# Kernel tuning notes

Measured on AMD Instinct MI355X. Metric: run time of the kernel, lower is better.

## Reference

```python
import jax, jax.numpy as jnp
import numpy as np

N, T, NC, D = 256, 20, 1, 32
NF, Q, VSTEPS, HDYN = 16, 32, 10, 256
HDIM = NF * 64           # n_filt * 4**3
DT = 0.1
BETA = 1.0
LOG2PI = float(np.log(2.0 * np.pi))


def conv2d(x, w, b):
    # k=4, s=2, p=1 : halves spatial dims. x: [B,Cin,H,W], w: [Cout,Cin,4,4]
    y = jax.lax.conv_general_dilated(x, w, (2, 2), [(1, 1), (1, 1)],
                                     dimension_numbers=('NCHW', 'OIHW', 'NCHW'))
    return y + b[None, :, None, None]


def deconv2d(x, w, b):
    # stride-2 transposed conv, doubles spatial dims. w: [Cout,Cin,4,4]
    y = jax.lax.conv_transpose(x, w, (2, 2), 'SAME',
                               dimension_numbers=('NCHW', 'OIHW', 'NCHW'))
    return y + b[None, :, None, None]


def encode(x, C1, c1, C2, c2, C3, c3, Wm, bm, Wl, bl):
    h = jax.nn.relu(conv2d(x, C1, c1))
    h = jax.nn.relu(conv2d(h, C2, c2))
    h = jax.nn.relu(conv2d(h, C3, c3))   # [B, 4*NF, 4, 4]
    h = h.reshape(h.shape[0], -1)        # [B, HDIM]
    return h @ Wm + bm, h @ Wl + bl


def setup_inputs() -> dict:
    key = jax.random.key(0)
    ks = jax.random.split(key, 40)
    r = lambda i, shape, s=0.05: s * jax.random.normal(ks[i], shape, jnp.float32)
    inp = {
        'X': jax.random.uniform(ks[0], (N, T, NC, D, D), jnp.float32),
        'eps_s0': jax.random.normal(ks[1], (N, Q), jnp.float32),
        'eps_v0': jax.random.normal(ks[2], (N, Q), jnp.float32),
        # enc_s (input = 1 frame)
        'Cs1': r(3, (NF, NC, 4, 4)), 'cs1': jnp.zeros((NF,)),
        'Cs2': r(4, (2 * NF, NF, 4, 4)), 'cs2': jnp.zeros((2 * NF,)),
        'Cs3': r(5, (4 * NF, 2 * NF, 4, 4)), 'cs3': jnp.zeros((4 * NF,)),
        'Wsm': r(6, (HDIM, Q)), 'bsm': jnp.zeros((Q,)),
        'Wsl': r(7, (HDIM, Q), 0.01), 'bsl': -1.0 * jnp.ones((Q,)),
        # enc_v (input = v_steps frames stacked as channels)
        'Cv1': r(8, (NF, VSTEPS * NC, 4, 4)), 'cv1': jnp.zeros((NF,)),
        'Cv2': r(9, (2 * NF, NF, 4, 4)), 'cv2': jnp.zeros((2 * NF,)),
        'Cv3': r(10, (4 * NF, 2 * NF, 4, 4)), 'cv3': jnp.zeros((4 * NF,)),
        'Wvm': r(11, (HDIM, Q)), 'bvm': jnp.zeros((Q,)),
        'Wvl': r(12, (HDIM, Q), 0.01), 'bvl': -1.0 * jnp.ones((Q,)),
        # dynamics f : R^{2q} -> R^q (tanh MLP)
        'W1': r(13, (2 * Q, HDYN), 0.1), 'b1': jnp.zeros((HDYN,)),
        'W2': r(14, (HDYN, Q), 0.1), 'b2': jnp.zeros((Q,)),
        # fc3 + decoder
        'Wf': r(15, (Q, HDIM)), 'bf': jnp.zeros((HDIM,)),
        'D1': r(16, (2 * NF, 4 * NF, 4, 4)), 'd1': jnp.zeros((2 * NF,)),
        'D2': r(17, (NF, 2 * NF, 4, 4)), 'd2': jnp.zeros((NF,)),
        'D3': r(18, (NC, NF, 4, 4)), 'd3': jnp.zeros((NC,)),
        'Ndata': 10000,
    }
    return inp


def reference(X, eps_s0, eps_v0,
              Cs1, cs1, Cs2, cs2, Cs3, cs3, Wsm, bsm, Wsl, bsl,
              Cv1, cv1, Cv2, cv2, Cv3, cv3, Wvm, bvm, Wvl, bvl,
              W1, b1, W2, b2, Wf, bf, D1, d1, D2, d2, D3, d3, Ndata):
    Nb, Tt = X.shape[0], X.shape[1]
    # ---- encode z0 = [v0, s0]
    s0_mu, s0_lv = encode(X[:, 0], Cs1, cs1, Cs2, cs2, Cs3, cs3, Wsm, bsm, Wsl, bsl)
    xv = X[:, :VSTEPS].reshape(Nb, VSTEPS * NC, D, D)
    v0_mu, v0_lv = encode(xv, Cv1, cv1, Cv2, cv2, Cv3, cv3, Wvm, bvm, Wvl, bvl)
    s0 = s0_mu + eps_s0 * jnp.exp(s0_lv)
    v0 = v0_mu + eps_v0 * jnp.exp(v0_lv)
    # standard-normal density of the base noise (q dims each)
    logp0 = (-0.5 * jnp.sum(eps_s0 ** 2, -1) - 0.5 * Q * LOG2PI) + \
            (-0.5 * jnp.sum(eps_v0 ** 2, -1) - 0.5 * Q * LOG2PI)
    z0 = jnp.concatenate([v0, s0], axis=1)               # [N,2q]
    qz0_m = jnp.concatenate([v0_mu, s0_mu], axis=1)
    qz0_logv = jnp.concatenate([v0_lv, s0_lv], axis=1)

    # ---- augmented ODE rhs: dz = [f(z), v], dlogp = -tr(df/dv)
    # exact trace for the tanh MLP: J = W2^T diag(1-h^2) W1^T, so
    # tr_{i<q} J = (1-h^2) @ c with c_k = sum_{i<q} W1[i,k] * W2[k,i]
    c = jnp.sum(W1[:Q] * W2.T, axis=0)                   # [HDYN]

    def rhs(vs):
        h = jnp.tanh(vs @ W1 + b1)                       # [N,HDYN]
        dv = h @ W2 + b2                                 # [N,q]
        dvs = jnp.concatenate([dv, vs[:, :Q]], axis=1)   # [N,2q]
        tr = (1.0 - h * h) @ c                           # [N]
        return dvs, -tr

    def rk4_step(carry, _):
        z, lp = carry
        k1z, k1l = rhs(z)
        k2z, k2l = rhs(z + 0.5 * DT * k1z)
        k3z, k3l = rhs(z + 0.5 * DT * k2z)
        k4z, k4l = rhs(z + DT * k3z)
        z2 = z + (DT / 6.0) * (k1z + 2 * k2z + 2 * k3z + k4z)
        lp2 = lp + (DT / 6.0) * (k1l + 2 * k2l + 2 * k3l + k4l)
        return (z2, lp2), (z2, lp2)

    (_, _), (zs, lps) = jax.lax.scan(rk4_step, (z0, logp0), None, length=Tt - 1)
    zt = jnp.concatenate([z0[None], zs], axis=0)         # [T,N,2q]
    logp = jnp.concatenate([logp0[None], lps], axis=0)   # [T,N]
    ztL = jnp.transpose(zt, (1, 0, 2))[None]             # [1,N,T,2q] (L=1)
    logpL = logp.T[None]                                 # [1,N,T]

    # ---- decode positions s_t
    s = ztL[..., Q:].reshape(-1, Q) @ Wf + bf            # [N*T, HDIM]
    h = s.reshape(-1, 4 * NF, 4, 4)
    h = jax.nn.relu(deconv2d(h, D1, d1))                 # [N*T,2NF,8,8]
    h = jax.nn.relu(deconv2d(h, D2, d2))                 # [N*T,NF,16,16]
    Xrec = jax.nn.sigmoid(deconv2d(h, D3, d3))           # [N*T,NC,32,32]
    Xrec = Xrec.reshape(1, Nb, Tt, NC, D, D)

    # ---- ELBO
    log_pzt = -0.5 * jnp.sum(ztL ** 2, -1) - Q * LOG2PI  # N(0,I) over 2q dims
    kl_z = (logpL - log_pzt).sum(2).mean(0)              # [N]
    lhood_L = jnp.log(0.001 + Xrec) * X[None] + jnp.log(1.001 - Xrec) * (1.0 - X[None])
    lhood = lhood_L.sum((2, 3, 4, 5)).mean(0)            # [N]
    kl_w = 0.5 * (jnp.sum(W1 ** 2) + jnp.sum(W2 ** 2))
    Nd = jnp.float32(Ndata)
    lh = Nd * lhood.mean()
    klz = Nd * kl_z.mean()
    elbo = lh - klz - BETA * kl_w
    return Xrec, qz0_m, qz0_logv, ztL, elbo, lh, klz, BETA * kl_w


if __name__ == '__main__':
    outs = reference(**setup_inputs())
    print(outs[0].shape, float(outs[4]))
```

## Files before the change

### kernel.cpp

```cpp
#include <hip/hip_runtime.h>
#include <math.h>

#define N_S 256
#define T_S 20
#define D_S 32
#define NF_S 16
#define Q_S 32
#define HDYN_S 256
#define HDIM_S 1024
#define VSTEPS_S 10
#define DT_S 0.1f
#define LOG2PI_F 1.8378770664093453f

#define OUT_XREC 0
#define OUT_QM   5242880
#define OUT_QLV  5259264
#define OUT_ZT   5275648
#define OUT_SCAL 5603328

#define OS_A1S   0
#define OS_A2S   1048576
#define OS_A3S   1572864

#define WS_A1V   0
#define WS_A3V   0
#define WS_WT2   32768
#define WS_WT3   40960
#define WS_A2V   1048576
#define WS_M1    1048576
#define WS_C1    1114112
#define WS_S0MU  1572864
#define WS_S0LV  1581056
#define WS_V0MU  1589248
#define WS_V0LV  1597440
#define WS_LOGP  1605632
#define WS_LHOOD 1610752
#define WS_KLZ   1611008
#define WS_KLW   1611264
#define WS_TC    1611520
#define TC_S1 (WS_TC + 0)
#define TC_V1 (WS_TC + 256)
#define TC_S2 (WS_TC + 2816)
#define TC_V2 (WS_TC + 11008)
#define TC_S3 (WS_TC + 19200)
#define TC_V3 (WS_TC + 51968)

__device__ inline void enc_tr(const float* __restrict__ src, float* __restrict__ dst,
                              int e, int CI, int CO) {
    int co = e % CO; int r = e / CO; int tap = r & 15; int ci = r >> 4;
    dst[e] = src[(co * CI + ci) * 16 + tap];
}
__device__ inline void dec_tr(const float* __restrict__ src, float* __restrict__ dst,
                              int e, int CI, int CO) {
    int co = e % CO; int r = e / CO; int ci = r % CI; int tap = r / CI;
    dst[e] = src[(co * CI + ci) * 16 + tap];
}

__global__ __launch_bounds__(256) void prep_enc(
    const float* __restrict__ Cs1, const float* __restrict__ Cv1,
    const float* __restrict__ Cs2, const float* __restrict__ Cv2,
    const float* __restrict__ Cs3, const float* __restrict__ Cv3,
    float* __restrict__ ws)
{
    int idx = blockIdx.x * 256 + threadIdx.x;
    if (blockIdx.x == 0) ws[WS_LHOOD + threadIdx.x] = 0.f;
    if (idx < 256)        enc_tr(Cs1, ws + TC_S1, idx,          1, 16);
    else if (idx < 2816)  enc_tr(Cv1, ws + TC_V1, idx - 256,   10, 16);
    else if (idx < 11008) enc_tr(Cs2, ws + TC_S2, idx - 2816,  16, 32);
    else if (idx < 19200) enc_tr(Cv2, ws + TC_V2, idx - 11008, 16, 32);
    else if (idx < 51968) enc_tr(Cs3, ws + TC_S3, idx - 19200, 32, 64);
    else if (idx < 84736) enc_tr(Cv3, ws + TC_V3, idx - 51968, 32, 64);
}

__global__ __launch_bounds__(256) void conv1_both(
    const float* __restrict__ x,
    const float* __restrict__ wts, const float* __restrict__ bs, float* __restrict__ outs,
    const float* __restrict__ wtv, const float* __restrict__ bv, float* __restrict__ outv)
{
    __shared__ float xin[10 * 630];
    int sel = blockIdx.z;
    int cin = sel ? 10 : 1;
    const float* wt = sel ? wtv : wts;
    const float* bias = sel ? bv : bs;
    float* out = sel ? outv : outs;

    int b = blockIdx.x, yh = blockIdx.y, t = threadIdx.x;
    for (int e = t; e < cin * 576; e += 256) {
        int ci = e / 576;
        int r = (e >> 5) - ci * 18;
        int cx = e & 31;
        int gy = yh * 16 - 1 + r;
        float v = (gy >= 0 && gy < 32) ? x[(size_t)b * 20480 + ci * 1024 + gy * 32 + cx] : 0.f;
        xin[ci * 630 + r * 35 + cx + 1] = v;
    }
    for (int e = t; e < cin * 18; e += 256) {
        int ci = e / 18, r = e - ci * 18;
        xin[ci * 630 + r * 35 + 0] = 0.f;
        xin[ci * 630 + r * 35 + 33] = 0.f;
    }
    __syncthreads();

    int ocq = __builtin_amdgcn_readfirstlane(t >> 7);
    int p = t & 127;
    int oyl = p >> 4, ox = p & 15;
    const float* wg = wt + ocq * 8;
    float acc[8];
    #pragma unroll
    for (int j = 0; j < 8; j++) acc[j] = bias[ocq * 8 + j];
    for (int ci = 0; ci < cin; ci++) {
        const float* xc = xin + ci * 630;
        const float* wc = wg + ci * 256;
        #pragma unroll
        for (int ky = 0; ky < 4; ky++) {
            const float* xr = xc + (2 * oyl + ky) * 35;
            #pragma unroll
            for (int kx = 0; kx < 4; kx++) {
                float v = xr[2 * ox + kx];
                const float4* w4 = (const float4*)(wc + (ky * 4 + kx) * 16);
                float4 wa = w4[0], wb2 = w4[1];
                acc[0] = fmaf(v, wa.x, acc[0]);
                acc[1] = fmaf(v, wa.y, acc[1]);
                acc[2] = fmaf(v, wa.z, acc[2]);
                acc[3] = fmaf(v, wa.w, acc[3]);
                acc[4] = fmaf(v, wb2.x, acc[4]);
                acc[5] = fmaf(v, wb2.y, acc[5]);
                acc[6] = fmaf(v, wb2.z, acc[6]);
                acc[7] = fmaf(v, wb2.w, acc[7]);
            }
        }
    }
    int oy = yh * 8 + oyl;
    size_t ob = (size_t)b * 4096 + (size_t)(ocq * 8) * 256 + oy * 16 + ox;
    #pragma unroll
    for (int j = 0; j < 8; j++) out[ob + (size_t)j * 256] = fmaxf(acc[j], 0.f);
}

__global__ __launch_bounds__(256) void conv2_both(
    const float* __restrict__ a1s, const float* __restrict__ wts, const float* __restrict__ bsb,
    float* __restrict__ outs,
    const float* __restrict__ a1v, const float* __restrict__ wtv, const float* __restrict__ bvb,
    float* __restrict__ outv)
{
    __shared__ float xin[16 * 272];
    int sel = blockIdx.z;
    const float* a1 = sel ? a1v : a1s;
    const float* wt = sel ? wtv : wts;
    const float* bias = sel ? bvb : bsb;
    float* out = sel ? outv : outs;

    int b = blockIdx.x, h = blockIdx.y, t = threadIdx.x;
    for (int e = t; e < 4096; e += 256) {
        int ci = e >> 8, r = e & 255, iy = r >> 4, ix = r & 15;
        xin[ci * 272 + iy * 17 + ix] = a1[(size_t)b * 4096 + e];
    }
    __syncthreads();

    int ocq = __builtin_amdgcn_readfirstlane(t >> 6);
    int p = t & 63;
    int pa = p >> 3, pb = p & 7;
    int hbase = h * 16 + ocq * 4;
    float acc[4];
    #pragma unroll
    for (int j = 0; j < 4; j++) acc[j] = bias[hbase + j];
    for (int ci = 0; ci < 16; ci++) {
        const float* xc = xin + ci * 272;
        const float* wc = wt + ci * 512 + hbase;
        #pragma unroll
        for (int ky = 0; ky < 4; ky++) {
            int iy = 2 * pa - 1 + ky;
            if ((unsigned)iy >= 16u) continue;
            const float* xr = xc + iy * 17;
            #pragma unroll
            for (int kx = 0; kx < 4; kx++) {
                int ix = 2 * pb - 1 + kx;
                if ((unsigned)ix >= 16u) continue;
                float v = xr[ix];
                float4 wv = *(const float4*)(wc + (ky * 4 + kx) * 32);
                acc[0] = fmaf(v, wv.x, acc[0]);
                acc[1] = fmaf(v, wv.y, acc[1]);
                acc[2] = fmaf(v, wv.z, acc[2]);
                acc[3] = fmaf(v, wv.w, acc[3]);
            }
        }
    }
    size_t ob = (size_t)b * 2048 + (size_t)(hbase) * 64 + pa * 8 + pb;
    #pragma unroll
    for (int j = 0; j < 4; j++) out[ob + (size_t)j * 64] = fmaxf(acc[j], 0.f);
}

__global__ __launch_bounds__(256) void conv3_both(
    const float* __restrict__ a2s, const float* __restrict__ wts, const float* __restrict__ bsb,
    float* __restrict__ outs,
    const float* __restrict__ a2v, const float* __restrict__ wtv, const float* __restrict__ bvb,
    float* __restrict__ outv)
{
    __shared__ float xin[32 * 72];
    __shared__ float wl[16384];
    __shared__ float bl[32];
    int sel = blockIdx.z;
    const float* a2 = sel ? a2v : a2s;
    const float* wt = sel ? wtv : wts;
    const float* bias = sel ? bvb : bsb;
    float* out = sel ? outv : outs;

    int b = blockIdx.x, h = blockIdx.y, t = threadIdx.x;
    for (int e = t; e < 2048; e += 256) {
        int ci = e >> 6, r = e & 63, iy = r >> 3, ix = r & 7;
        xin[ci * 72 + iy * 9 + ix] = a2[(size_t)b * 2048 + e];
    }
    for (int e4 = t; e4 < 4096; e4 += 256) {
        int grp = e4 >> 3, c4 = e4 & 7;
        ((float4*)wl)[e4] = ((const float4*)(wt + grp * 64 + h * 32))[c4];
    }
    if (t < 32) bl[t] = bias[h * 32 + t];
    __syncthreads();

    int ocq = t >> 4, p = t & 15;
    int pa = p >> 2, pb = p & 3;
    float a0 = bl[ocq * 2], a1 = bl[ocq * 2 + 1];
    for (int ci = 0; ci < 32; ci++) {
        const float* xc = xin + ci * 72;
        const float* wc = wl + ci * 512 + ocq * 2;
        #pragma unroll
        for (int ky = 0; ky < 4; ky++) {
            int iy = 2 * pa - 1 + ky;
            if ((unsigned)iy >= 8u) continue;
            const float* xr = xc + iy * 9;
            #pragma unroll
            for (int kx = 0; kx < 4; kx++) {
                int ix = 2 * pb - 1 + kx;
                if ((unsigned)ix >= 8u) continue;
                float v = xr[ix];
                float2 wv = *(const float2*)(wc + (ky * 4 + kx) * 32);
                a0 = fmaf(v, wv.x, a0);
                a1 = fmaf(v, wv.y, a1);
            }
        }
    }
    size_t ob = (size_t)b * 1024 + (size_t)(h * 32 + ocq * 2) * 16 + pa * 4 + pb;
    out[ob] = fmaxf(a0, 0.f);
    out[ob + 16] = fmaxf(a1, 0.f);
}

__global__ __launch_bounds__(256) void fc_both(
    const float* __restrict__ hs, const float* __restrict__ hv,
    const float* __restrict__ Wsm, const float* __restrict__ bsm,
    const float* __restrict__ Wsl, const float* __restrict__ bsl,
    const float* __restrict__ Wvm, const float* __restrict__ bvm,
    const float* __restrict__ Wvl, const float* __restrict__ bvl,
    float* __restrict__ mus, float* __restrict__ lvs,
    float* __restrict__ muv, float* __restrict__ lvv)
{
    __shared__ float pm[8][32], pl[8][32];
    int sel = blockIdx.x >> 8;
    int b = blockIdx.x & 255, t = threadIdx.x;
    const float* h  = sel ? hv : hs;
    const float* Wm = sel ? Wvm : Wsm;
    const float* bm = sel ? bvm : bsm;
    const float* Wl = sel ? Wvl : Wsl;
    const float* bl = sel ? bvl : bsl;
    float* mu = sel ? muv : mus;
    float* lv = sel ? lvv : lvs;

    int q = t & 31, c = t >> 5;
    const float* hb = h + (size_t)b * HDIM_S + c * 128;
    const float* wmp = Wm + (c * 128) * Q_S + q;
    const float* wlp = Wl + (c * 128) * Q_S + q;
    float am = 0.f, al = 0.f;
    #pragma unroll 4
    for (int k = 0; k < 128; k++) {
        float hv2 = hb[k];
        am = fmaf(hv2, wmp[k * Q_S], am);
        al = fmaf(hv2, wlp[k * Q_S], al);
    }
    pm[c][q] = am; pl[c][q] = al;
    __syncthreads();
    if (t < 32) {
        float s = bm[t];
        #pragma unroll
        for (int c2 = 0; c2 < 8; c2++) s += pm[c2][t];
        mu[b * Q_S + t] = s;
    } else if (t < 64) {
        int qq = t - 32;
        float s = bl[qq];
        #pragma unroll
        for (int c2 = 0; c2 < 8; c2++) s += pl[c2][qq];
        lv[b * Q_S + qq] = s;
    }
}

__global__ __launch_bounds__(256) void reparam_prep(
    const float* __restrict__ s0mu, const float* __restrict__ s0lv,
    const float* __restrict__ v0mu, const float* __restrict__ v0lv,
    const float* __restrict__ eps_s, const float* __restrict__ eps_v,
    const float* __restrict__ Wf, const float* __restrict__ bf,
    const float* __restrict__ D1, const float* __restrict__ d1,
    const float* __restrict__ D2, const float* __restrict__ D3,
    float* __restrict__ ws,
    float* __restrict__ qm, float* __restrict__ qlv,
    float* __restrict__ ztL, float* __restrict__ logp)
{
    __shared__ float shA[4096];
    __shared__ float shB[4096];
    int n = blockIdx.x, t = threadIdx.x;

    if (n < 64) {
        int j = n >> 3, q4 = n & 7;
        for (int e = t; e < 4096; e += 256) {
            int qq = e >> 10, k = e & 1023;
            shA[e] = Wf[(size_t)(q4 * 4 + qq) * 1024 + k];
        }
        for (int e = t; e < 4096; e += 256) {
            int ocg = e >> 10, r = e & 1023;
            shB[e] = D1[(size_t)(ocg * 8 + j) * 1024 + r];
        }
        __syncthreads();
        int p = t & 63, ocg = t >> 6;
        int y = p >> 3, x = p & 7;
        float acc[4] = {0.f, 0.f, 0.f, 0.f};
        #pragma unroll
        for (int sy = 0; sy < 2; sy++) {
            int ky = (y & 1) + 2 * sy;
            int iy = ((y + ky) >> 1) - 1;
            if ((unsigned)iy >= 4u) continue;
            #pragma unroll
            for (int sx = 0; sx < 2; sx++) {
                int kx = (x & 1) + 2 * sx;
                int ix = ((x + kx) >> 1) - 1;
                if ((unsigned)ix >= 4u) continue;
                const float* dl = shB + ocg * 1024 + ky * 4 + kx;
                const float* wl = shA + iy * 4 + ix;
                for (int ci = 0; ci < 64; ci++) {
                    float wv = dl[ci * 16];
                    int kb = ci * 16;
                    acc[0] = fmaf(wl[kb],        wv, acc[0]);
                    acc[1] = fmaf(wl[1024 + kb], wv, acc[1]);
                    acc[2] = fmaf(wl[2048 + kb], wv, acc[2]);
                    acc[3] = fmaf(wl[3072 + kb], wv, acc[3]);
                }
            }
        }
        ((float4*)(ws + WS_M1))[n * 256 + t] = make_float4(acc[0], acc[1], acc[2], acc[3]);
    } else if (n < 80) {
        int bb = n - 64;
        for (int e = t; e < 1024; e += 256) shA[e] = bf[e];
        for (int e = t; e < 2048; e += 256) shB[e] = D1[(size_t)bb * 2048 + e];
        __syncthreads();
        int oidx = t >> 1, half = t & 1;
        int ocr = oidx >> 6, p = oidx & 63;
        int y = p >> 3, x = p & 7;
        float acc = 0.f;
        #pragma unroll
        for (int sy = 0; sy < 2; sy++) {
            int ky = (y & 1) + 2 * sy;
            int iy = ((y + ky) >> 1) - 1;
            if ((unsigned)iy >= 4u) continue;
            #pragma unroll
            for (int sx = 0; sx < 2; sx++) {
                int kx = (x & 1) + 2 * sx;
                int ix = ((x + kx) >> 1) - 1;
                if ((unsigned)ix >= 4u) continue;
                const float* dl = shB + ocr * 1024 + half * 512 + ky * 4 + kx;
                const float* wl = shA + half * 512 + iy * 4 + ix;
                for (int cc = 0; cc < 32; cc++)
                    acc = fmaf(wl[cc * 16], dl[cc * 16], acc);
            }
        }
        acc += __shfl_down(acc, 1, 64);
        if (half == 0) {
            int oc = bb * 2 + ocr;
            ws[WS_C1 + (oc & 7) * 256 + (oc >> 3) * 64 + p] = acc + d1[oc];
        }
    } else if (n < 113) {
        int idx = (n - 80) * 256 + t;
        if (idx < 8192)      dec_tr(D2, ws + WS_WT2, idx,        32, 16);
        else if (idx < 8448) dec_tr(D3, ws + WS_WT3, idx - 8192, 16, 1);
    }

    if (t < 64) {
        int q = t & 31;
        float mu, lvv2, ep;
        if (t < 32) { mu = v0mu[n*32+q]; lvv2 = v0lv[n*32+q]; ep = eps_v[n*32+q]; }
        else        { mu = s0mu[n*32+q]; lvv2 = s0lv[n*32+q]; ep = eps_s[n*32+q]; }
        float zv = fmaf(ep, expf(lvv2), mu);
        qm[n*64 + t]  = mu;
        qlv[n*64 + t] = lvv2;
        ztL[(size_t)n * T_S * 64 + t] = zv;
        float e2 = ep * ep;
        #pragma unroll
        for (int off = 32; off; off >>= 1) e2 += __shfl_down(e2, off, 64);
        if (t == 0) logp[n * T_S] = -0.5f * e2 - Q_S * LOG2PI_F;
    }
}

__global__ __launch_bounds__(256) void ode_kernel(
    const float* __restrict__ W1, const float* __restrict__ b1,
    const float* __restrict__ W2, const float* __restrict__ b2,
    float* __restrict__ ztL, const float* __restrict__ logp,
    float* __restrict__ klz)
{
    __shared__ float W2s[HDYN_S * Q_S];
    __shared__ float zeval[64];
    __shared__ float hsh[HDYN_S];
    __shared__ float dvred[HDYN_S];
    __shared__ float red4[4];
    int n = blockIdx.x;
    int t = threadIdx.x;

    for (int i = t; i < HDYN_S * Q_S; i += 256) W2s[i] = W2[i];
    float w1r[64];
    #pragma unroll
    for (int j = 0; j < 64; j++) w1r[j] = W1[j * HDYN_S + t];
    float b1r = b1[t];
    __syncthreads();
    float ck = 0.f;
    #pragma unroll
    for (int i = 0; i < Q_S; i++) ck = fmaf(w1r[i], W2s[t * Q_S + i], ck);

    size_t zoff = (size_t)n * T_S * 64;
    float zj = 0.f, ksumj = 0.f, zevalj = 0.f, lp = 0.f, lsum = 0.f, klacc = 0.f;
    if (t < 64) { zj = ztL[zoff + t]; zevalj = zj; zeval[t] = zj; }
    if (t == 0) lp = logp[n * T_S];

    if (t < 64) {
        float e2 = zj * zj;
        #pragma unroll
        for (int off = 32; off; off >>= 1) e2 += __shfl_down(e2, off, 64);
        if (t == 0) klacc += lp - (-0.5f * e2 - Q_S * LOG2PI_F);
    }

    const float wc[4] = {1.f, 2.f, 2.f, 1.f};
    const float ac[3] = {0.5f * DT_S, 0.5f * DT_S, DT_S};

    for (int step = 1; step < T_S; step++) {
        for (int e = 0; e < 4; e++) {
            __syncthreads();
            float p0 = 0.f, p1 = 0.f, p2 = 0.f, p3 = 0.f;
            #pragma unroll
            for (int j = 0; j < 16; j++) {
                p0 = fmaf(zeval[j],      w1r[j],      p0);
                p1 = fmaf(zeval[j + 16], w1r[j + 16], p1);
                p2 = fmaf(zeval[j + 32], w1r[j + 32], p2);
                p3 = fmaf(zeval[j + 48], w1r[j + 48], p3);
            }
            float pre = b1r + ((p0 + p1) + (p2 + p3));
            float hk = tanhf(pre);
            hsh[t] = hk;
            float gk = (1.f - hk * hk) * ck;
            #pragma unroll
            for (int off = 32; off; off >>= 1) gk += __shfl_down(gk, off, 64);
            if ((t & 63) == 0) red4[t >> 6] = gk;
            __syncthreads();
            {
                int i = t & 31, p = t >> 5;
                float a0 = 0.f, a1 = 0.f;
                #pragma unroll
                for (int kk = 0; kk < 16; kk++) {
                    a0 = fmaf(hsh[p * 32 + kk],      W2s[(p * 32 + kk) * Q_S + i],      a0);
                    a1 = fmaf(hsh[p * 32 + 16 + kk], W2s[(p * 32 + 16 + kk) * Q_S + i], a1);
                }
                dvred[t] = a0 + a1;
            }
            __syncthreads();
            if (t < 64) {
                float tr = red4[0] + red4[1] + red4[2] + red4[3];
                float zv_shfl = __shfl(zevalj, (t >= 32) ? (t - 32) : t, 64);
                float kzv;
                if (t < 32) {
                    float dvi = b2[t];
                    #pragma unroll
                    for (int p = 0; p < 8; p++) dvi += dvred[p * 32 + t];
                    kzv = dvi;
                } else kzv = zv_shfl;
                if (e == 0) ksumj = kzv; else ksumj = fmaf(wc[e], kzv, ksumj);
                if (t == 0) { float kl = -tr; lsum = (e == 0) ? kl : fmaf(wc[e], kl, lsum); }
                if (e < 3) {
                    zevalj = fmaf(ac[e], kzv, zj);
                    zeval[t] = zevalj;
                } else {
                    zj = fmaf(DT_S / 6.f, ksumj, zj);
                    zevalj = zj; zeval[t] = zj;
                    ztL[zoff + step * 64 + t] = zj;
                    if (t == 0) lp = fmaf(DT_S / 6.f, lsum, lp);
                    float e2 = zj * zj;
                    #pragma unroll
                    for (int off = 32; off; off >>= 1) e2 += __shfl_down(e2, off, 64);
                    if (t == 0) klacc += lp - (-0.5f * e2 - Q_S * LOG2PI_F);
                }
            }
        }
    }
    if (t == 0) klz[n] = klacc;
}

__global__ __launch_bounds__(256) void decoder5(
    const float* __restrict__ ztL, const float* __restrict__ M1L, const float* __restrict__ c1L,
    const float* __restrict__ wt2, const float* __restrict__ d2,
    const float* __restrict__ wt3, const float* __restrict__ d3,
    const float* __restrict__ X, float* __restrict__ Xrec, float* __restrict__ lhood)
{
    __shared__ float zs[32];
    __shared__ float regA[3600];
    __shared__ float regB[4160];
    __shared__ float sh4[4];
    float* h2f = regB;
    float* h1f = regA;
    float* xst = regA;
    const int bidx = blockIdx.x;
    const int t = threadIdx.x;
    const int wu = __builtin_amdgcn_readfirstlane(t >> 6);
    const int l = t & 63;
    const int py = wu >> 1, px = wu & 1;

    if (t < 32) zs[t] = ztL[(size_t)bidx * 64 + 32 + t];
    {
        float4 z4 = make_float4(0.f, 0.f, 0.f, 0.f);
        for (int e = t; e < 900; e += 256) ((float4*)regA)[e] = z4;
    }
    __syncthreads();

    {
        float acc[8];
        #pragma unroll
        for (int j = 0; j < 8; j++) acc[j] = c1L[j * 256 + t];
        const float4* M14 = (const float4*)M1L;
        #pragma unroll
        for (int q4 = 0; q4 < 8; q4++) {
            float4 z4 = *(const float4*)(zs + q4 * 4);
            #pragma unroll
            for (int j = 0; j < 8; j++) {
                float4 m = M14[(j * 8 + q4) * 256 + t];
                acc[j] = fmaf(z4.x, m.x, fmaf(z4.y, m.y, fmaf(z4.z, m.z, fmaf(z4.w, m.w, acc[j]))));
            }
        }
        int p = t & 63, ocg = t >> 6;
        int y = p >> 3, x = p & 7;
        float* hp = h1f + (y + 1) * 360 + (x + 1) * 36 + ocg * 8;
        float4 r0, r1;
        r0.x = fmaxf(acc[0], 0.f); r0.y = fmaxf(acc[1], 0.f);
        r0.z = fmaxf(acc[2], 0.f); r0.w = fmaxf(acc[3], 0.f);
        r1.x = fmaxf(acc[4], 0.f); r1.y = fmaxf(acc[5], 0.f);
        r1.z = fmaxf(acc[6], 0.f); r1.w = fmaxf(acc[7], 0.f);
        *(float4*)(hp)     = r0;
        *(float4*)(hp + 4) = r1;
    }
    __syncthreads();

    {
        int a = l >> 3, b = l & 7;
        float acc[16];
        #pragma unroll
        for (int j = 0; j < 16; j++) acc[j] = d2[j];
        #pragma unroll
        for (int sy = 0; sy < 2; sy++) {
            int ky = py + 2 * sy;
            int iyf = a + py + sy - 1;
            #pragma unroll
            for (int sx = 0; sx < 2; sx++) {
                int kx = px + 2 * sx;
                int ixf = b + px + sx - 1;
                const float4* ip4 = (const float4*)(h1f + (iyf + 1) * 360 + (ixf + 1) * 36);
                const float* wb = wt2 + (ky * 4 + kx) * 512;
                #pragma unroll 2
                for (int cc = 0; cc < 8; cc++) {
                    float4 v = ip4[cc];
                    float vv[4] = {v.x, v.y, v.z, v.w};
                    #pragma unroll
                    for (int r = 0; r < 4; r++) {
                        const float4* wq = (const float4*)(wb + (cc * 4 + r) * 16);
                        float4 w0 = wq[0], w1 = wq[1], w2 = wq[2], w3 = wq[3];
                        float vr = vv[r];
                        acc[0]  = fmaf(vr, w0.x, acc[0]);
                        acc[1]  = fmaf(vr, w0.y, acc[1]);
                        acc[2]  = fmaf(vr, w0.z, acc[2]);
                        acc[3]  = fmaf(vr, w0.w, acc[3]);
                        acc[4]  = fmaf(vr, w1.x, acc[4]);
                        acc[5]  = fmaf(vr, w1.y, acc[5]);
                        acc[6]  = fmaf(vr, w1.z, acc[6]);
                        acc[7]  = fmaf(vr, w1.w, acc[7]);
                        acc[8]  = fmaf(vr, w2.x, acc[8]);
                        acc[9]  = fmaf(vr, w2.y, acc[9]);
                        acc[10] = fmaf(vr, w2.z, acc[10]);
                        acc[11] = fmaf(vr, w2.w, acc[11]);
                        acc[12] = fmaf(vr, w3.x, acc[12]);
                        acc[13] = fmaf(vr, w3.y, acc[13]);
                        acc[14] = fmaf(vr, w3.z, acc[14]);
                        acc[15] = fmaf(vr, w3.w, acc[15]);
                    }
                }
            }
        }
        float* hq = h2f + (2 * a + py) * 260 + (2 * b + px) * 16;
        #pragma unroll
        for (int j = 0; j < 4; j++) {
            float4 r;
            r.x = fmaxf(acc[j*4+0], 0.f);
            r.y = fmaxf(acc[j*4+1], 0.f);
            r.z = fmaxf(acc[j*4+2], 0.f);
            r.w = fmaxf(acc[j*4+3], 0.f);
            *(float4*)(hq + j * 4) = r;
        }
    }
    __syncthreads();

    {
        int oy2 = l >> 2, b3 = l & 3;
        float acc[4];
        float d30 = d3[0];
        #pragma unroll
        for (int k = 0; k < 4; k++) acc[k] = d30;
        #pragma unroll
        for (int sy = 0; sy < 2; sy++) {
            int ky = py + 2 * sy;
            int iy = oy2 + py + sy - 1;
            if ((unsigned)iy >= 16u) continue;
            #pragma unroll
            for (int sx = 0; sx < 2; sx++) {
                int kx = px + 2 * sx;
                int cx = px + sx - 1;
                const float* wvp = wt3 + (ky * 4 + kx) * 16;
                #pragma unroll
                for (int k = 0; k < 4; k++) {
                    int ix = b3 + 4 * k + cx;
                    if ((unsigned)ix >= 16u) continue;
                    const float4* in4 = (const float4*)(h2f + iy * 260 + ix * 16);
                    #pragma unroll
                    for (int cc = 0; cc < 4; cc++) {
                        float4 v = in4[cc];
                        float4 wq = ((const float4*)wvp)[cc];
                        acc[k] = fmaf(v.x, wq.x, acc[k]);
                        acc[k] = fmaf(v.y, wq.y, acc[k]);
                        acc[k] = fmaf(v.z, wq.z, acc[k]);
                        acc[k] = fmaf(v.w, wq.w, acc[k]);
                    }
                }
            }
        }
        int oy = 2 * oy2 + py;
        #pragma unroll
        for (int k = 0; k < 4; k++) {
            int ox = 2 * (b3 + 4 * k) + px;
            xst[oy * 36 + ox] = 1.f / (1.f + expf(-acc[k]));
        }
    }
    __syncthreads();

    {
        int row = t >> 3, col = (t & 7) * 4;
        float4 xr4 = *(const float4*)(xst + row * 36 + col);
        *(float4*)(Xrec + (size_t)bidx * 1024 + t * 4) = xr4;
        float4 xi4 = *(const float4*)(X + (size_t)bidx * 1024 + t * 4);
        float ll = 0.f;
        ll += logf(0.001f + xr4.x) * xi4.x + logf(1.001f - xr4.x) * (1.f - xi4.x);
        ll += logf(0.001f + xr4.y) * xi4.y + logf(1.001f - xr4.y) * (1.f - xi4.y);
        ll += logf(0.001f + xr4.z) * xi4.z + logf(1.001f - xr4.z) * (1.f - xi4.z);
        ll += logf(0.001f + xr4.w) * xi4.w + logf(1.001f - xr4.w) * (1.f - xi4.w);
        #pragma unroll
        for (int off = 32; off; off >>= 1) ll += __shfl_down(ll, off, 64);
        if ((t & 63) == 0) sh4[t >> 6] = ll;
    }
    __syncthreads();
    if (t == 0) atomicAdd(&lhood[bidx / T_S], sh4[0] + sh4[1] + sh4[2] + sh4[3]);
}

__global__ __launch_bounds__(256) void final2(
    const float* __restrict__ lhood, const float* __restrict__ klz,
    const float* __restrict__ W1, const float* __restrict__ W2,
    const int* __restrict__ Ndata, float* __restrict__ outs)
{
    __shared__ float shA[4], shB[4], shC[4];
    int t = threadIdx.x;
    float a = lhood[t];
    float b = klz[t];
    float c = 0.f;
    for (int i = t; i < 64 * HDYN_S; i += 256) c = fmaf(W1[i], W1[i], c);
    for (int i = t; i < HDYN_S * Q_S; i += 256) c = fmaf(W2[i], W2[i], c);
    #pragma unroll
    for (int off = 32; off; off >>= 1) {
        a += __shfl_down(a, off, 64);
        b += __shfl_down(b, off, 64);
        c += __shfl_down(c, off, 64);
    }
    if ((t & 63) == 0) { shA[t >> 6] = a; shB[t >> 6] = b; shC[t >> 6] = c; }
    __syncthreads();
    if (t == 0) {
        float Nd = (float)Ndata[0];
        float lh = Nd * ((shA[0] + shA[1] + shA[2] + shA[3]) / 256.f);
        float kz = Nd * ((shB[0] + shB[1] + shB[2] + shB[3]) / 256.f);
        float bkw = 0.5f * (shC[0] + shC[1] + shC[2] + shC[3]);
        outs[0] = lh - kz - bkw;
        outs[1] = lh;
        outs[2] = kz;
        outs[3] = bkw;
    }
}

extern "C" void kernel_launch(void* const* d_in, const int* in_sizes, int n_in,
                              void* d_out, int out_size, void* d_ws, size_t ws_size,
                              hipStream_t stream) {
    const float* X      = (const float*)d_in[0];
    const float* eps_s0 = (const float*)d_in[1];
    const float* eps_v0 = (const float*)d_in[2];
    const float* Cs1 = (const float*)d_in[3],  *cs1 = (const float*)d_in[4];
    const float* Cs2 = (const float*)d_in[5],  *cs2 = (const float*)d_in[6];
    const float* Cs3 = (const float*)d_in[7],  *cs3 = (const float*)d_in[8];
    const float* Wsm = (const float*)d_in[9],  *bsm = (const float*)d_in[10];
    const float* Wsl = (const float*)d_in[11], *bsl = (const float*)d_in[12];
    const float* Cv1 = (const float*)d_in[13], *cv1 = (const float*)d_in[14];
    const float* Cv2 = (const float*)d_in[15], *cv2 = (const float*)d_in[16];
    const float* Cv3 = (const float*)d_in[17], *cv3 = (const float*)d_in[18];
    const float* Wvm = (const float*)d_in[19], *bvm = (const float*)d_in[20];
    const float* Wvl = (const float*)d_in[21], *bvl = (const float*)d_in[22];
    const float* W1  = (const float*)d_in[23], *b1  = (const float*)d_in[24];
    const float* W2  = (const float*)d_in[25], *b2  = (const float*)d_in[26];
    const float* Wf  = (const float*)d_in[27], *bf  = (const float*)d_in[28];
    const float* D1  = (const float*)d_in[29], *d1  = (const float*)d_in[30];
    const float* D2  = (const float*)d_in[31], *d2  = (const float*)d_in[32];
    const float* D3  = (const float*)d_in[33], *d3  = (const float*)d_in[34];
    const int*   Ndata = (const int*)d_in[35];

    float* out = (float*)d_out;
    float* ws  = (float*)d_ws;

    float* a1s = out + OS_A1S;
    float* a2s = out + OS_A2S;
    float* a3s = out + OS_A3S;

    prep_enc<<<331, 256, 0, stream>>>(Cs1, Cv1, Cs2, Cv2, Cs3, Cv3, ws);

    conv1_both<<<dim3(256, 2, 2), 256, 0, stream>>>(X,
        ws + TC_S1, cs1, a1s,
        ws + TC_V1, cv1, ws + WS_A1V);
    conv2_both<<<dim3(256, 2, 2), 256, 0, stream>>>(
        a1s, ws + TC_S2, cs2, a2s,
        ws + WS_A1V, ws + TC_V2, cv2, ws + WS_A2V);
    conv3_both<<<dim3(256, 2, 2), 256, 0, stream>>>(
        a2s, ws + TC_S3, cs3, a3s,
        ws + WS_A2V, ws + TC_V3, cv3, ws + WS_A3V);
    fc_both<<<512, 256, 0, stream>>>(a3s, ws + WS_A3V,
        Wsm, bsm, Wsl, bsl, Wvm, bvm, Wvl, bvl,
        ws + WS_S0MU, ws + WS_S0LV, ws + WS_V0MU, ws + WS_V0LV);

    reparam_prep<<<256, 256, 0, stream>>>(ws + WS_S0MU, ws + WS_S0LV, ws + WS_V0MU, ws + WS_V0LV,
                                          eps_s0, eps_v0, Wf, bf, D1, d1, D2, D3, ws,
                                          out + OUT_QM, out + OUT_QLV,
                                          out + OUT_ZT, ws + WS_LOGP);

    ode_kernel<<<256, 256, 0, stream>>>(W1, b1, W2, b2, out + OUT_ZT, ws + WS_LOGP,
                                        ws + WS_KLZ);

    decoder5<<<5120, 256, 0, stream>>>(out + OUT_ZT, ws + WS_M1, ws + WS_C1,
                                       ws + WS_WT2, d2, ws + WS_WT3, d3,
                                       X, out + OUT_XREC, ws + WS_LHOOD);

    final2<<<1, 256, 0, stream>>>(ws + WS_LHOOD, ws + WS_KLZ, W1, W2, Ndata,
                                  out + OUT_SCAL);
}
```

Baseline: 495.3 us.

## Fuse conv3 with FC heads and fold reparam/decoder prep into ODE launch

```diff
diff --git a/kernel.cpp b/kernel.cpp
--- a/kernel.cpp
+++ b/kernel.cpp
@@ -20,10 +20,8 @@
 
 #define OS_A1S   0
 #define OS_A2S   1048576
-#define OS_A3S   1572864
 
 #define WS_A1V   0
-#define WS_A3V   0
 #define WS_WT2   32768
 #define WS_WT3   40960
 #define WS_A2V   1048576
@@ -33,10 +31,8 @@
 #define WS_S0LV  1581056
 #define WS_V0MU  1589248
 #define WS_V0LV  1597440
-#define WS_LOGP  1605632
 #define WS_LHOOD 1610752
 #define WS_KLZ   1611008
-#define WS_KLW   1611264
 #define WS_TC    1611520
 #define TC_S1 (WS_TC + 0)
 #define TC_V1 (WS_TC + 256)
@@ -62,14 +58,20 @@
     const float* __restrict__ Cs3, const float* __restrict__ Cv3,
     float* __restrict__ ws)
 {
-    int idx = blockIdx.x * 256 + threadIdx.x;
-    if (blockIdx.x == 0) ws[WS_LHOOD + threadIdx.x] = 0.f;
-    if (idx < 256)        enc_tr(Cs1, ws + TC_S1, idx,          1, 16);
-    else if (idx < 2816)  enc_tr(Cv1, ws + TC_V1, idx - 256,   10, 16);
-    else if (idx < 11008) enc_tr(Cs2, ws + TC_S2, idx - 2816,  16, 32);
-    else if (idx < 19200) enc_tr(Cv2, ws + TC_V2, idx - 11008, 16, 32);
-    else if (idx < 51968) enc_tr(Cs3, ws + TC_S3, idx - 19200, 32, 64);
-    else if (idx < 84736) enc_tr(Cv3, ws + TC_V3, idx - 51968, 32, 64);
+    int blk = blockIdx.x, t = threadIdx.x;
+    if (blk < 331) {
+        int idx = blk * 256 + t;
+        if (blk == 0) ws[WS_LHOOD + t] = 0.f;
+        if (idx < 256)        enc_tr(Cs1, ws + TC_S1, idx,          1, 16);
+        else if (idx < 2816)  enc_tr(Cv1, ws + TC_V1, idx - 256,   10, 16);
+        else if (idx < 11008) enc_tr(Cs2, ws + TC_S2, idx - 2816,  16, 32);
+        else if (idx < 19200) enc_tr(Cv2, ws + TC_V2, idx - 11008, 16, 32);
+        else if (idx < 51968) enc_tr(Cs3, ws + TC_S3, idx - 19200, 32, 64);
+        else if (idx < 84736) enc_tr(Cv3, ws + TC_V3, idx - 51968, 32, 64);
+    } else {
+        int zi = (blk - 331) * 256 + t;
+        ws[WS_S0MU + zi] = 0.f;
+    }
 }
 
 __global__ __launch_bounds__(256) void conv1_both(
@@ -188,20 +190,25 @@
     for (int j = 0; j < 4; j++) out[ob + (size_t)j * 64] = fmaxf(acc[j], 0.f);
 }
 
-__global__ __launch_bounds__(256) void conv3_both(
-    const float* __restrict__ a2s, const float* __restrict__ wts, const float* __restrict__ bsb,
-    float* __restrict__ outs,
-    const float* __restrict__ a2v, const float* __restrict__ wtv, const float* __restrict__ bvb,
-    float* __restrict__ outv)
+__global__ __launch_bounds__(256) void conv3fc_both(
+    const float* __restrict__ a2s, const float* __restrict__ wts,
+    const float* __restrict__ bsb,
+    const float* __restrict__ Wsm, const float* __restrict__ Wsl,
+    float* __restrict__ mus, float* __restrict__ lvs,
+    const float* __restrict__ a2v, const float* __restrict__ wtv,
+    const float* __restrict__ bvb,
+    const float* __restrict__ Wvm, const float* __restrict__ Wvl,
+    float* __restrict__ muv, float* __restrict__ lvv)
 {
     __shared__ float xin[32 * 72];
     __shared__ float wl[16384];
     __shared__ float bl[32];
+    __shared__ float hbuf[512];
+    __shared__ float pr[256];
     int sel = blockIdx.z;
     const float* a2 = sel ? a2v : a2s;
     const float* wt = sel ? wtv : wts;
     const float* bias = sel ? bvb : bsb;
-    float* out = sel ? outv : outs;
 
     int b = blockIdx.x, h = blockIdx.y, t = threadIdx.x;
     for (int e = t; e < 2048; e += 256) {
@@ -237,167 +244,43 @@
             }
         }
     }
-    size_t ob = (size_t)b * 1024 + (size_t)(h * 32 + ocq * 2) * 16 + pa * 4 + pb;
-    out[ob] = fmaxf(a0, 0.f);
-    out[ob + 16] = fmaxf(a1, 0.f);
-}
-
-__global__ __launch_bounds__(256) void fc_both(
-    const float* __restrict__ hs, const float* __restrict__ hv,
-    const float* __restrict__ Wsm, const float* __restrict__ bsm,
-    const float* __restrict__ Wsl, const float* __restrict__ bsl,
-    const float* __restrict__ Wvm, const float* __restrict__ bvm,
-    const float* __restrict__ Wvl, const float* __restrict__ bvl,
-    float* __restrict__ mus, float* __restrict__ lvs,
-    float* __restrict__ muv, float* __restrict__ lvv)
-{
-    __shared__ float pm[8][32], pl[8][32];
-    int sel = blockIdx.x >> 8;
-    int b = blockIdx.x & 255, t = threadIdx.x;
-    const float* h  = sel ? hv : hs;
-    const float* Wm = sel ? Wvm : Wsm;
-    const float* bm = sel ? bvm : bsm;
-    const float* Wl = sel ? Wvl : Wsl;
-    const float* bl = sel ? bvl : bsl;
-    float* mu = sel ? muv : mus;
-    float* lv = sel ? lvv : lvs;
-
-    int q = t & 31, c = t >> 5;
-    const float* hb = h + (size_t)b * HDIM_S + c * 128;
-    const float* wmp = Wm + (c * 128) * Q_S + q;
-    const float* wlp = Wl + (c * 128) * Q_S + q;
-    float am = 0.f, al = 0.f;
-    #pragma unroll 4
-    for (int k = 0; k < 128; k++) {
-        float hv2 = hb[k];
-        am = fmaf(hv2, wmp[k * Q_S], am);
-        al = fmaf(hv2, wlp[k * Q_S], al);
-    }
-    pm[c][q] = am; pl[c][q] = al;
-    __syncthreads();
-    if (t < 32) {
-        float s = bm[t];
-        #pragma unroll
-        for (int c2 = 0; c2 < 8; c2++) s += pm[c2][t];
-        mu[b * Q_S + t] = s;
-    } else if (t < 64) {
-        int qq = t - 32;
-        float s = bl[qq];
-        #pragma unroll
-        for (int c2 = 0; c2 < 8; c2++) s += pl[c2][qq];
-        lv[b * Q_S + qq] = s;
-    }
-}
-
-__global__ __launch_bounds__(256) void reparam_prep(
-    const float* __restrict__ s0mu, const float* __restrict__ s0lv,
-    const float* __restrict__ v0mu, const float* __restrict__ v0lv,
+    int lp_ = ocq * 32 + p;
+    hbuf[lp_]      = fmaxf(a0, 0.f);
+    hbuf[lp_ + 16] = fmaxf(a1, 0.f);
+    __syncthreads();
+
+    {
+        int q = t & 63, c = t >> 6, qq = q & 31;
+        const float* Wb = (q < 32) ? (sel ? Wvm : Wsm) : (sel ? Wvl : Wsl);
+        const float* wp = Wb + (size_t)(h * 512 + c * 128) * 32 + qq;
+        const float* hp = hbuf + c * 128;
+        float s = 0.f;
+        #pragma unroll 4
+        for (int k = 0; k < 128; k++) s = fmaf(hp[k], wp[(size_t)k * 32], s);
+        pr[c * 64 + q] = s;
+    }
+    __syncthreads();
+    if (t < 64) {
+        float s = (pr[t] + pr[64 + t]) + (pr[128 + t] + pr[192 + t]);
+        float* dst = (t < 32) ? (sel ? muv : mus) : (sel ? lvv : lvs);
+        atomicAdd(&dst[b * 32 + (t & 31)], s);
+    }
+}
+
+__global__ __launch_bounds__(256) void ode_kernel(
+    const float* __restrict__ W1, const float* __restrict__ b1,
+    const float* __restrict__ W2, const float* __restrict__ b2,
+    const float* __restrict__ s0mu_a, const float* __restrict__ s0lv_a,
+    const float* __restrict__ v0mu_a, const float* __restrict__ v0lv_a,
+    const float* __restrict__ bsm, const float* __restrict__ bsl,
+    const float* __restrict__ bvm, const float* __restrict__ bvl,
     const float* __restrict__ eps_s, const float* __restrict__ eps_v,
     const float* __restrict__ Wf, const float* __restrict__ bf,
     const float* __restrict__ D1, const float* __restrict__ d1,
     const float* __restrict__ D2, const float* __restrict__ D3,
     float* __restrict__ ws,
     float* __restrict__ qm, float* __restrict__ qlv,
-    float* __restrict__ ztL, float* __restrict__ logp)
-{
-    __shared__ float shA[4096];
-    __shared__ float shB[4096];
-    int n = blockIdx.x, t = threadIdx.x;
-
-    if (n < 64) {
-        int j = n >> 3, q4 = n & 7;
-        for (int e = t; e < 4096; e += 256) {
-            int qq = e >> 10, k = e & 1023;
-            shA[e] = Wf[(size_t)(q4 * 4 + qq) * 1024 + k];
-        }
-        for (int e = t; e < 4096; e += 256) {
-            int ocg = e >> 10, r = e & 1023;
-            shB[e] = D1[(size_t)(ocg * 8 + j) * 1024 + r];
-        }
-        __syncthreads();
-        int p = t & 63, ocg = t >> 6;
-        int y = p >> 3, x = p & 7;
-        float acc[4] = {0.f, 0.f, 0.f, 0.f};
-        #pragma unroll
-        for (int sy = 0; sy < 2; sy++) {
-            int ky = (y & 1) + 2 * sy;
-            int iy = ((y + ky) >> 1) - 1;
-            if ((unsigned)iy >= 4u) continue;
-            #pragma unroll
-            for (int sx = 0; sx < 2; sx++) {
-                int kx = (x & 1) + 2 * sx;
-                int ix = ((x + kx) >> 1) - 1;
-                if ((unsigned)ix >= 4u) continue;
-                const float* dl = shB + ocg * 1024 + ky * 4 + kx;
-                const float* wl = shA + iy * 4 + ix;
-                for (int ci = 0; ci < 64; ci++) {
-                    float wv = dl[ci * 16];
-                    int kb = ci * 16;
-                    acc[0] = fmaf(wl[kb],        wv, acc[0]);
-                    acc[1] = fmaf(wl[1024 + kb], wv, acc[1]);
-                    acc[2] = fmaf(wl[2048 + kb], wv, acc[2]);
-                    acc[3] = fmaf(wl[3072 + kb], wv, acc[3]);
-                }
-            }
-        }
-        ((float4*)(ws + WS_M1))[n * 256 + t] = make_float4(acc[0], acc[1], acc[2], acc[3]);
-    } else if (n < 80) {
-        int bb = n - 64;
-        for (int e = t; e < 1024; e += 256) shA[e] = bf[e];
-        for (int e = t; e < 2048; e += 256) shB[e] = D1[(size_t)bb * 2048 + e];
-        __syncthreads();
-        int oidx = t >> 1, half = t & 1;
-        int ocr = oidx >> 6, p = oidx & 63;
-        int y = p >> 3, x = p & 7;
-        float acc = 0.f;
-        #pragma unroll
-        for (int sy = 0; sy < 2; sy++) {
-            int ky = (y & 1) + 2 * sy;
-            int iy = ((y + ky) >> 1) - 1;
-            if ((unsigned)iy >= 4u) continue;
-            #pragma unroll
-            for (int sx = 0; sx < 2; sx++) {
-                int kx = (x & 1) + 2 * sx;
-                int ix = ((x + kx) >> 1) - 1;
-                if ((unsigned)ix >= 4u) continue;
-                const float* dl = shB + ocr * 1024 + half * 512 + ky * 4 + kx;
-                const float* wl = shA + half * 512 + iy * 4 + ix;
-                for (int cc = 0; cc < 32; cc++)
-                    acc = fmaf(wl[cc * 16], dl[cc * 16], acc);
-            }
-        }
-        acc += __shfl_down(acc, 1, 64);
-        if (half == 0) {
-            int oc = bb * 2 + ocr;
-            ws[WS_C1 + (oc & 7) * 256 + (oc >> 3) * 64 + p] = acc + d1[oc];
-        }
-    } else if (n < 113) {
-        int idx = (n - 80) * 256 + t;
-        if (idx < 8192)      dec_tr(D2, ws + WS_WT2, idx,        32, 16);
-        else if (idx < 8448) dec_tr(D3, ws + WS_WT3, idx - 8192, 16, 1);
-    }
-
-    if (t < 64) {
-        int q = t & 31;
-        float mu, lvv2, ep;
-        if (t < 32) { mu = v0mu[n*32+q]; lvv2 = v0lv[n*32+q]; ep = eps_v[n*32+q]; }
-        else        { mu = s0mu[n*32+q]; lvv2 = s0lv[n*32+q]; ep = eps_s[n*32+q]; }
-        float zv = fmaf(ep, expf(lvv2), mu);
-        qm[n*64 + t]  = mu;
-        qlv[n*64 + t] = lvv2;
-        ztL[(size_t)n * T_S * 64 + t] = zv;
-        float e2 = ep * ep;
-        #pragma unroll
-        for (int off = 32; off; off >>= 1) e2 += __shfl_down(e2, off, 64);
-        if (t == 0) logp[n * T_S] = -0.5f * e2 - Q_S * LOG2PI_F;
-    }
-}
-
-__global__ __launch_bounds__(256) void ode_kernel(
-    const float* __restrict__ W1, const float* __restrict__ b1,
-    const float* __restrict__ W2, const float* __restrict__ b2,
-    float* __restrict__ ztL, const float* __restrict__ logp,
-    float* __restrict__ klz)
+    float* __restrict__ ztL, float* __restrict__ klz)
 {
     __shared__ float W2s[HDYN_S * Q_S];
     __shared__ float zeval[64];
@@ -407,6 +290,85 @@
     int n = blockIdx.x;
     int t = threadIdx.x;
 
+    if (n >= 256) {
+        float* shA = W2s;
+        float* shB = W2s + 4096;
+        int m = n - 256;
+        if (m < 64) {
+            int j = m >> 3, q4 = m & 7;
+            for (int e = t; e < 4096; e += 256) {
+                int qq = e >> 10, k = e & 1023;
+                shA[e] = Wf[(size_t)(q4 * 4 + qq) * 1024 + k];
+            }
+            for (int e = t; e < 4096; e += 256) {
+                int ocg = e >> 10, r = e & 1023;
+                shB[e] = D1[(size_t)(ocg * 8 + j) * 1024 + r];
+            }
+            __syncthreads();
+            int p = t & 63, ocg = t >> 6;
+            int y = p >> 3, x = p & 7;
+            float acc[4] = {0.f, 0.f, 0.f, 0.f};
+            #pragma unroll
+            for (int sy = 0; sy < 2; sy++) {
+                int ky = (y & 1) + 2 * sy;
+                int iy = ((y + ky) >> 1) - 1;
+                if ((unsigned)iy >= 4u) continue;
+                #pragma unroll
+                for (int sx = 0; sx < 2; sx++) {
+                    int kx = (x & 1) + 2 * sx;
+                    int ix = ((x + kx) >> 1) - 1;
+                    if ((unsigned)ix >= 4u) continue;
+                    const float* dl = shB + ocg * 1024 + ky * 4 + kx;
+                    const float* wl = shA + iy * 4 + ix;
+                    for (int ci = 0; ci < 64; ci++) {
+                        float wv = dl[ci * 16];
+                        int kb = ci * 16;
+                        acc[0] = fmaf(wl[kb],        wv, acc[0]);
+                        acc[1] = fmaf(wl[1024 + kb], wv, acc[1]);
+                        acc[2] = fmaf(wl[2048 + kb], wv, acc[2]);
+                        acc[3] = fmaf(wl[3072 + kb], wv, acc[3]);
+                    }
+                }
+            }
+            ((float4*)(ws + WS_M1))[m * 256 + t] = make_float4(acc[0], acc[1], acc[2], acc[3]);
+        } else if (m < 80) {
+            int bb = m - 64;
+            for (int e = t; e < 1024; e += 256) shA[e] = bf[e];
+            for (int e = t; e < 2048; e += 256) shB[e] = D1[(size_t)bb * 2048 + e];
+            __syncthreads();
+            int oidx = t >> 1, half = t & 1;
+            int ocr = oidx >> 6, p = oidx & 63;
+            int y = p >> 3, x = p & 7;
+            float acc = 0.f;
+            #pragma unroll
+            for (int sy = 0; sy < 2; sy++) {
+                int ky = (y & 1) + 2 * sy;
+                int iy = ((y + ky) >> 1) - 1;
+                if ((unsigned)iy >= 4u) continue;
+                #pragma unroll
+                for (int sx = 0; sx < 2; sx++) {
+                    int kx = (x & 1) + 2 * sx;
+                    int ix = ((x + kx) >> 1) - 1;
+                    if ((unsigned)ix >= 4u) continue;
+                    const float* dl = shB + ocr * 1024 + half * 512 + ky * 4 + kx;
+                    const float* wl = shA + half * 512 + iy * 4 + ix;
+                    for (int cc = 0; cc < 32; cc++)
+                        acc = fmaf(wl[cc * 16], dl[cc * 16], acc);
+                }
+            }
+            acc += __shfl_down(acc, 1, 64);
+            if (half == 0) {
+                int oc = bb * 2 + ocr;
+                ws[WS_C1 + (oc & 7) * 256 + (oc >> 3) * 64 + p] = acc + d1[oc];
+            }
+        } else {
+            int idx = (m - 80) * 256 + t;
+            if (idx < 8192)      dec_tr(D2, ws + WS_WT2, idx,        32, 16);
+            else if (idx < 8448) dec_tr(D3, ws + WS_WT3, idx - 8192, 16, 1);
+        }
+        return;
+    }
+
     for (int i = t; i < HDYN_S * Q_S; i += 256) W2s[i] = W2[i];
     float w1r[64];
     #pragma unroll
@@ -419,29 +381,57 @@
 
     size_t zoff = (size_t)n * T_S * 64;
     float zj = 0.f, ksumj = 0.f, zevalj = 0.f, lp = 0.f, lsum = 0.f, klacc = 0.f;
-    if (t < 64) { zj = ztL[zoff + t]; zevalj = zj; zeval[t] = zj; }
-    if (t == 0) lp = logp[n * T_S];
 
     if (t < 64) {
-        float e2 = zj * zj;
-        #pragma unroll
-        for (int off = 32; off; off >>= 1) e2 += __shfl_down(e2, off, 64);
-        if (t == 0) klacc += lp - (-0.5f * e2 - Q_S * LOG2PI_F);
+        int q = t & 31;
+        float mu, lvv2, ep;
+        if (t < 32) { mu = v0mu_a[n*32+q] + bvm[q]; lvv2 = v0lv_a[n*32+q] + bvl[q]; ep = eps_v[n*32+q]; }
+        else        { mu = s0mu_a[n*32+q] + bsm[q]; lvv2 = s0lv_a[n*32+q] + bsl[q]; ep = eps_s[n*32+q]; }
+        float zv = fmaf(ep, expf(lvv2), mu);
+        qm[n*64 + t]  = mu;
+        qlv[n*64 + t] = lvv2;
+        zj = zv; zevalj = zv; zeval[t] = zv;
+        ztL[zoff + t] = zv;
+        float e2 = ep * ep;
+        float z2 = zv * zv;
+        #pragma unroll
+        for (int off = 32; off; off >>= 1) {
+            e2 += __shfl_down(e2, off, 64);
+            z2 += __shfl_down(z2, off, 64);
+        }
+        if (t == 0) {
+            lp = -0.5f * e2 - Q_S * LOG2PI_F;
+            klacc = lp - (-0.5f * z2 - Q_S * LOG2PI_F);
+        }
     }
 
     const float wc[4] = {1.f, 2.f, 2.f, 1.f};
     const float ac[3] = {0.5f * DT_S, 0.5f * DT_S, DT_S};
+    const float4* ze4 = (const float4*)zeval;
 
     for (int step = 1; step < T_S; step++) {
         for (int e = 0; e < 4; e++) {
             __syncthreads();
             float p0 = 0.f, p1 = 0.f, p2 = 0.f, p3 = 0.f;
             #pragma unroll
-            for (int j = 0; j < 16; j++) {
-                p0 = fmaf(zeval[j],      w1r[j],      p0);
-                p1 = fmaf(zeval[j + 16], w1r[j + 16], p1);
-                p2 = fmaf(zeval[j + 32], w1r[j + 32], p2);
-                p3 = fmaf(zeval[j + 48], w1r[j + 48], p3);
+            for (int j4 = 0; j4 < 4; j4++) {
+                float4 za = ze4[j4], zb = ze4[4 + j4], zc = ze4[8 + j4], zd = ze4[12 + j4];
+                p0 = fmaf(za.x, w1r[j4*4+0], p0);
+                p0 = fmaf(za.y, w1r[j4*4+1], p0);
+                p0 = fmaf(za.z, w1r[j4*4+2], p0);
+                p0 = fmaf(za.w, w1r[j4*4+3], p0);
+                p1 = fmaf(zb.x, w1r[16+j4*4+0], p1);
+                p1 = fmaf(zb.y, w1r[16+j4*4+1], p1);
+                p1 = fmaf(zb.z, w1r[16+j4*4+2], p1);
+                p1 = fmaf(zb.w, w1r[16+j4*4+3], p1);
+                p2 = fmaf(zc.x, w1r[32+j4*4+0], p2);
+                p2 = fmaf(zc.y, w1r[32+j4*4+1], p2);
+                p2 = fmaf(zc.z, w1r[32+j4*4+2], p2);
+                p2 = fmaf(zc.w, w1r[32+j4*4+3], p2);
+                p3 = fmaf(zd.x, w1r[48+j4*4+0], p3);
+                p3 = fmaf(zd.y, w1r[48+j4*4+1], p3);
+                p3 = fmaf(zd.z, w1r[48+j4*4+2], p3);
+                p3 = fmaf(zd.w, w1r[48+j4*4+3], p3);
             }
             float pre = b1r + ((p0 + p1) + (p2 + p3));
             float hk = tanhf(pre);
@@ -453,11 +443,22 @@
             __syncthreads();
             {
                 int i = t & 31, p = t >> 5;
+                const float4* h4 = (const float4*)(hsh + p * 32);
                 float a0 = 0.f, a1 = 0.f;
                 #pragma unroll
-                for (int kk = 0; kk < 16; kk++) {
-                    a0 = fmaf(hsh[p * 32 + kk],      W2s[(p * 32 + kk) * Q_S + i],      a0);
-                    a1 = fmaf(hsh[p * 32 + 16 + kk], W2s[(p * 32 + 16 + kk) * Q_S + i], a1);
+                for (int kk4 = 0; kk4 < 4; kk4++) {
+                    float4 ha = h4[kk4];
+                    float4 hb2 = h4[4 + kk4];
+                    int kb = p * 32 + kk4 * 4;
+                    a0 = fmaf(ha.x, W2s[(kb+0)*Q_S + i], a0);
+                    a0 = fmaf(ha.y, W2s[(kb+1)*Q_S + i], a0);
+                    a0 = fmaf(ha.z, W2s[(kb+2)*Q_S + i], a0);
+                    a0 = fmaf(ha.w, W2s[(kb+3)*Q_S + i], a0);
+                    int kc = kb + 16;
+                    a1 = fmaf(hb2.x, W2s[(kc+0)*Q_S + i], a1);
+                    a1 = fmaf(hb2.y, W2s[(kc+1)*Q_S + i], a1);
+                    a1 = fmaf(hb2.z, W2s[(kc+2)*Q_S + i], a1);
+                    a1 = fmaf(hb2.w, W2s[(kc+3)*Q_S + i], a1);
                 }
                 dvred[t] = a0 + a1;
             }
@@ -482,10 +483,10 @@
                     zevalj = zj; zeval[t] = zj;
                     ztL[zoff + step * 64 + t] = zj;
                     if (t == 0) lp = fmaf(DT_S / 6.f, lsum, lp);
-                    float e2 = zj * zj;
+                    float z2 = zj * zj;
                     #pragma unroll
-                    for (int off = 32; off; off >>= 1) e2 += __shfl_down(e2, off, 64);
-                    if (t == 0) klacc += lp - (-0.5f * e2 - Q_S * LOG2PI_F);
+                    for (int off = 32; off; off >>= 1) z2 += __shfl_down(z2, off, 64);
+                    if (t == 0) klacc += lp - (-0.5f * z2 - Q_S * LOG2PI_F);
                 }
             }
         }
@@ -724,9 +725,8 @@
 
     float* a1s = out + OS_A1S;
     float* a2s = out + OS_A2S;
-    float* a3s = out + OS_A3S;
-
-    prep_enc<<<331, 256, 0, stream>>>(Cs1, Cv1, Cs2, Cv2, Cs3, Cv3, ws);
+
+    prep_enc<<<459, 256, 0, stream>>>(Cs1, Cv1, Cs2, Cv2, Cs3, Cv3, ws);
 
     conv1_both<<<dim3(256, 2, 2), 256, 0, stream>>>(X,
         ws + TC_S1, cs1, a1s,
@@ -734,20 +734,15 @@
     conv2_both<<<dim3(256, 2, 2), 256, 0, stream>>>(
         a1s, ws + TC_S2, cs2, a2s,
         ws + WS_A1V, ws + TC_V2, cv2, ws + WS_A2V);
-    conv3_both<<<dim3(256, 2, 2), 256, 0, stream>>>(
-        a2s, ws + TC_S3, cs3, a3s,
-        ws + WS_A2V, ws + TC_V3, cv3, ws + WS_A3V);
-    fc_both<<<512, 256, 0, stream>>>(a3s, ws + WS_A3V,
-        Wsm, bsm, Wsl, bsl, Wvm, bvm, Wvl, bvl,
-        ws + WS_S0MU, ws + WS_S0LV, ws + WS_V0MU, ws + WS_V0LV);
-
-    reparam_prep<<<256, 256, 0, stream>>>(ws + WS_S0MU, ws + WS_S0LV, ws + WS_V0MU, ws + WS_V0LV,
-                                          eps_s0, eps_v0, Wf, bf, D1, d1, D2, D3, ws,
-                                          out + OUT_QM, out + OUT_QLV,
-                                          out + OUT_ZT, ws + WS_LOGP);
-
-    ode_kernel<<<256, 256, 0, stream>>>(W1, b1, W2, b2, out + OUT_ZT, ws + WS_LOGP,
-                                        ws + WS_KLZ);
+    conv3fc_both<<<dim3(256, 2, 2), 256, 0, stream>>>(
+        a2s, ws + TC_S3, cs3, Wsm, Wsl, ws + WS_S0MU, ws + WS_S0LV,
+        ws + WS_A2V, ws + TC_V3, cv3, Wvm, Wvl, ws + WS_V0MU, ws + WS_V0LV);
+
+    ode_kernel<<<369, 256, 0, stream>>>(W1, b1, W2, b2,
+        ws + WS_S0MU, ws + WS_S0LV, ws + WS_V0MU, ws + WS_V0LV,
+        bsm, bsl, bvm, bvl, eps_s0, eps_v0,
+        Wf, bf, D1, d1, D2, D3, ws,
+        out + OUT_QM, out + OUT_QLV, out + OUT_ZT, ws + WS_KLZ);
 
     decoder5<<<5120, 256, 0, stream>>>(out + OUT_ZT, ws + WS_M1, ws + WS_C1,
                                        ws + WS_WT2, d2, ws + WS_WT3, d3,
```

Result: no change. 488.6 us (-1.4%).
